# Performance work log

Measured on AMD Instinct MI355X. Metric: run time of the kernel, lower is better.

The kernel has to match this reference:

```python
import jax, jax.numpy as jnp
import numpy as np

EPS = 1e-5

def _pairwise_sq_dist(x, e):
    # x: [N, D], e: [M, D] -> [N, M]; matches torch.addmm(||e||^2 + ||x||^2, x, e.T, alpha=-2, beta=1)
    return (jnp.sum(e * e, axis=1)[None, :]
            + jnp.sum(x * x, axis=1, keepdims=True)
            - 2.0 * (x @ e.T))

def _dist2ph(d, t):
    # softmax(-sqrt(d)/t); clamp tiny negative numerical residues before sqrt
    return jax.nn.softmax(-jnp.sqrt(jnp.maximum(d, 0.0)) / t, axis=-1)

def setup_inputs() -> dict:
    key = jax.random.key(0)
    k1, k2, k3 = jax.random.split(key, 3)
    B, T, D, M = 64, 128, 256, 1024
    audio_semantic = jax.random.normal(k1, (B, T, D), dtype=jnp.float32)
    video_semantic = jax.random.normal(k2, (B, T, D), dtype=jnp.float32)
    init_bound = 1.0 / 400.0
    embedding = jax.random.uniform(k3, (M, D), dtype=jnp.float32,
                                   minval=-init_bound, maxval=init_bound)
    return {"audio_semantic": audio_semantic,
            "video_semantic": video_semantic,
            "embedding": embedding}

def reference(audio_semantic, video_semantic, embedding):
    B, T, D = audio_semantic.shape
    M = embedding.shape[0]
    emb_sg = jax.lax.stop_gradient(embedding)

    # ---- VQ argmin + straight-through quantize (Audio/Video_vq_embedding) ----
    a_flat_sg = jax.lax.stop_gradient(audio_semantic).reshape(-1, D)
    v_flat_sg = jax.lax.stop_gradient(video_semantic).reshape(-1, D)
    a_idx = jnp.argmin(_pairwise_sq_dist(a_flat_sg, emb_sg), axis=-1)  # [B*T]
    v_idx = jnp.argmin(_pairwise_sq_dist(v_flat_sg, emb_sg), axis=-1)
    a_quantized = audio_semantic + jax.lax.stop_gradient(
        emb_sg[a_idx].reshape(B, T, D) - audio_semantic)
    v_quantized = video_semantic + jax.lax.stop_gradient(
        emb_sg[v_idx].reshape(B, T, D) - video_semantic)

    # ---- entropy-weighted cross-modal contrastive loss (cmcm_loss) ----
    a_dg = _pairwise_sq_dist(audio_semantic.reshape(-1, D), embedding)  # [B*T, M], grads flow
    v_dg = _pairwise_sq_dist(video_semantic.reshape(-1, D), embedding)

    a_pH = _dist2ph(a_dg, 1.0).reshape(B, T, M).transpose(1, 0, 2)     # [T, B, M]
    v_pH = _dist2ph(v_dg, 1.0).reshape(B, T, M).transpose(1, 0, 2)
    a_adj_ph = _dist2ph(a_dg, 0.5).reshape(B, T, M).transpose(1, 0, 2)
    v_adj_ph = _dist2ph(v_dg, 0.5).reshape(B, T, M).transpose(1, 0, 2)

    def cmcm(p_adj, q):
        # Scode[t] = p_adj[t] @ log(q[t]).T  -> [T, B, B]
        S = jnp.einsum('tbm,tcm->tbc', p_adj, jnp.log(q + 1e-10))
        S = S + jnp.max(-S)                 # matches MaxScode = max(-Scode)
        E = jnp.exp(S)
        diag = jnp.diagonal(E, axis1=-2, axis2=-1)          # [T, B]
        return -jnp.mean(jnp.log(diag / (jnp.sum(E, axis=-1) + EPS)))

    Lcmcm = cmcm(a_adj_ph, v_pH)
    Lcmcm2 = cmcm(v_adj_ph, a_pH)
    cmcm_loss = 0.5 * (Lcmcm + Lcmcm2)
    return cmcm_loss, a_quantized, v_quantized
```

## Files before the change

kernel.cpp:

```cpp
#include <hip/hip_runtime.h>

#define NROWS 8192
#define MCB   1024
#define DD    256
#define TT    128
#define BB    64

#define OFF_DA      0ul
#define OFF_DV      8388608ul
#define OFF_XX_A    16777216ul
#define OFF_XX_V    16785408ul
#define OFF_EE      16793600ul
#define OFF_SMIN_A  16794624ul
#define OFF_LZ1_A   16802816ul
#define OFF_IZ2_A   16811008ul
#define OFF_IDX_A   16819200ul
#define OFF_SMIN_V  16827392ul
#define OFF_LZ1_V   16835584ul
#define OFF_IZ2_V   16843776ul
#define OFF_IDX_V   16851968ul
#define OFF_S1      16860160ul
#define OFF_S2      17384448ul
#define OFF_PART    17908736ul
#define OFF_MAX     17908992ul
#define OFF_PACC    17909000ul
#define OFF_HIA     17909504ul
#define OFF_LOA     (OFF_HIA + 1048576ul)
#define OFF_HIV     (OFF_HIA + 2097152ul)
#define OFF_LOV     (OFF_HIA + 3145728ul)
#define OFF_HIE     (OFF_HIA + 4194304ul)
#define OFF_LOE     (OFF_HIE + 131072ul)

typedef __attribute__((ext_vector_type(8))) short bf16x8;
typedef __attribute__((ext_vector_type(4))) float f32x4;

__device__ __forceinline__ void gload_lds16u(const ushort* gsrc, ushort* ldst) {
  __builtin_amdgcn_global_load_lds(
      (const __attribute__((address_space(1))) void*)gsrc,
      (__attribute__((address_space(3))) void*)ldst, 16, 0, 0);
}
__device__ __forceinline__ ushort bf16_rne(float x) {
  unsigned u = __float_as_uint(x);
  unsigned r = u + 0x7FFFu + ((u >> 16) & 1u);
  return (ushort)(r >> 16);
}
__device__ __forceinline__ float bf16_f(ushort h) {
  return __uint_as_float((unsigned)h << 16);
}

__global__ void k_sumsq(const float* __restrict__ A, const float* __restrict__ V,
                        const float* __restrict__ E, float* __restrict__ ws) {
  const int lane = threadIdx.x & 63;
  const int wid  = threadIdx.x >> 6;
  const int row = blockIdx.x * 4 + wid;
  const float* src; float* dst; ushort* hi; ushort* lo; int r;
  if (row < 8192)       { src = A; r = row;         dst = ws + OFF_XX_A;
                          hi = (ushort*)(ws + OFF_HIA); lo = (ushort*)(ws + OFF_LOA); }
  else if (row < 16384) { src = V; r = row - 8192;  dst = ws + OFF_XX_V;
                          hi = (ushort*)(ws + OFF_HIV); lo = (ushort*)(ws + OFF_LOV); }
  else                  { src = E; r = row - 16384; dst = ws + OFF_EE;
                          hi = (ushort*)(ws + OFF_HIE); lo = (ushort*)(ws + OFF_LOE); }
  float4 x = *(const float4*)(src + (size_t)r * DD + lane * 4);
  ushort4 h, l;
  h.x = bf16_rne(x.x); l.x = bf16_rne(x.x - bf16_f(h.x));
  h.y = bf16_rne(x.y); l.y = bf16_rne(x.y - bf16_f(h.y));
  h.z = bf16_rne(x.z); l.z = bf16_rne(x.z - bf16_f(h.z));
  h.w = bf16_rne(x.w); l.w = bf16_rne(x.w - bf16_f(h.w));
  *(ushort4*)(hi + (size_t)r * DD + lane * 4) = h;
  *(ushort4*)(lo + (size_t)r * DD + lane * 4) = l;
  double acc = (double)x.x * x.x + (double)x.y * x.y +
               (double)x.z * x.z + (double)x.w * x.w;
  #pragma unroll
  for (int off = 32; off; off >>= 1) acc += __shfl_xor(acc, off);
  if (lane == 0) dst[r] = (float)acc;
}

__global__ __launch_bounds__(256) void k_dist(const float* __restrict__ A,
    const float* __restrict__ V, const float* __restrict__ E,
    float* __restrict__ ws) {
  const int z = blockIdx.z;
  const ushort* Xhi = (const ushort*)(ws + (z ? OFF_HIV : OFF_HIA));
  const ushort* Xlo = (const ushort*)(ws + (z ? OFF_LOV : OFF_LOA));
  const ushort* Ehi = (const ushort*)(ws + OFF_HIE);
  const ushort* Elo = (const ushort*)(ws + OFF_LOE);
  const float* xx = ws + (z ? OFF_XX_V : OFF_XX_A);
  const float* ee = ws + OFF_EE;
  float* Dst = ws + (z ? OFF_DV : OFF_DA);

  __shared__ __align__(16) ushort LAhi[128 * 32];
  __shared__ __align__(16) ushort LAlo[128 * 32];
  __shared__ __align__(16) ushort LBhi[128 * 32];
  __shared__ __align__(16) ushort LBlo[128 * 32];

  const int tid = threadIdx.x;
  const int bid = blockIdx.y * 8 + blockIdx.x;
  const int sw  = (bid & 7) * 64 + (bid >> 3);
  const int colb = sw & 7, rowb = sw >> 3;
  const int row0 = rowb * 128;
  const int col0 = colb * 128;

  const int wv = tid >> 6, lane = tid & 63;
  const int wr = wv >> 1, wc = wv & 1;
  const int rl = lane & 15, kg = lane >> 4;

  const int c0 = tid, c1 = 256 + tid;
  const int r0 = c0 >> 2, lg0 = (c0 & 3) ^ ((r0 >> 1) & 3);
  const int r1 = c1 >> 2, lg1 = (c1 & 3) ^ ((r1 >> 1) & 3);
  const ushort* gAhi0 = Xhi + (size_t)(row0 + r0) * DD + lg0 * 8;
  const ushort* gAhi1 = Xhi + (size_t)(row0 + r1) * DD + lg1 * 8;
  const ushort* gAlo0 = Xlo + (size_t)(row0 + r0) * DD + lg0 * 8;
  const ushort* gAlo1 = Xlo + (size_t)(row0 + r1) * DD + lg1 * 8;
  const ushort* gBhi0 = Ehi + (size_t)(col0 + r0) * DD + lg0 * 8;
  const ushort* gBhi1 = Ehi + (size_t)(col0 + r1) * DD + lg1 * 8;
  const ushort* gBlo0 = Elo + (size_t)(col0 + r0) * DD + lg0 * 8;
  const ushort* gBlo1 = Elo + (size_t)(col0 + r1) * DD + lg1 * 8;
  const int d0 = c0 * 8, d1 = c1 * 8;

  int aidx[4], bidx[4];
  #pragma unroll
  for (int f = 0; f < 4; ++f) {
    int ra = wr * 64 + f * 16 + rl;
    aidx[f] = ra * 32 + ((kg ^ ((ra >> 1) & 3)) << 3);
    int rb = wc * 64 + f * 16 + rl;
    bidx[f] = rb * 32 + ((kg ^ ((rb >> 1) & 3)) << 3);
  }

  f32x4 acc[4][4] = {};

  for (int t = 0; t < 8; ++t) {
    const int kc = t * 32;
    gload_lds16u(gAhi0 + kc, &LAhi[d0]);
    gload_lds16u(gAhi1 + kc, &LAhi[d1]);
    gload_lds16u(gAlo0 + kc, &LAlo[d0]);
    gload_lds16u(gAlo1 + kc, &LAlo[d1]);
    gload_lds16u(gBhi0 + kc, &LBhi[d0]);
    gload_lds16u(gBhi1 + kc, &LBhi[d1]);
    gload_lds16u(gBlo0 + kc, &LBlo[d0]);
    gload_lds16u(gBlo1 + kc, &LBlo[d1]);
    __syncthreads();
    __builtin_amdgcn_s_setprio(1);
    bf16x8 ahi[4], alo[4], bhi[4], blo[4];
    #pragma unroll
    for (int f = 0; f < 4; ++f) {
      ahi[f] = *(const bf16x8*)(&LAhi[aidx[f]]);
      alo[f] = *(const bf16x8*)(&LAlo[aidx[f]]);
      bhi[f] = *(const bf16x8*)(&LBhi[bidx[f]]);
      blo[f] = *(const bf16x8*)(&LBlo[bidx[f]]);
    }
    #pragma unroll
    for (int fr = 0; fr < 4; ++fr)
      #pragma unroll
      for (int fc = 0; fc < 4; ++fc) {
        acc[fr][fc] = __builtin_amdgcn_mfma_f32_16x16x32_bf16(
            ahi[fr], bhi[fc], acc[fr][fc], 0, 0, 0);
        acc[fr][fc] = __builtin_amdgcn_mfma_f32_16x16x32_bf16(
            ahi[fr], blo[fc], acc[fr][fc], 0, 0, 0);
        acc[fr][fc] = __builtin_amdgcn_mfma_f32_16x16x32_bf16(
            alo[fr], bhi[fc], acc[fr][fc], 0, 0, 0);
      }
    __builtin_amdgcn_s_setprio(0);
    __syncthreads();
  }

  float xn[4][4];
  #pragma unroll
  for (int fr = 0; fr < 4; ++fr)
    #pragma unroll
    for (int v = 0; v < 4; ++v)
      xn[fr][v] = xx[row0 + wr * 64 + fr * 16 + kg * 4 + v];
  #pragma unroll
  for (int fc = 0; fc < 4; ++fc) {
    const int m = col0 + wc * 64 + fc * 16 + rl;
    const float em = ee[m];
    #pragma unroll
    for (int fr = 0; fr < 4; ++fr) {
      #pragma unroll
      for (int v = 0; v < 4; ++v) {
        const int n = row0 + wr * 64 + fr * 16 + kg * 4 + v;
        Dst[(size_t)n * MCB + m] = (em + xn[fr][v]) - 2.0f * acc[fr][fc][v];
      }
    }
  }
}

__global__ void k_rowstats(const float* __restrict__ A, const float* __restrict__ V,
                           const float* __restrict__ E, float* __restrict__ ws,
                           float* __restrict__ out) {
  const int z = blockIdx.y;
  float* Dm = ws + (z ? OFF_DV : OFF_DA);
  const float* X  = z ? V : A;
  float* smin_o = ws + (z ? OFF_SMIN_V : OFF_SMIN_A);
  float* lz1_o  = ws + (z ? OFF_LZ1_V  : OFF_LZ1_A);
  float* iz2_o  = ws + (z ? OFF_IZ2_V  : OFF_IZ2_A);
  int*   idx_o  = (int*)(ws + (z ? OFF_IDX_V : OFF_IDX_A));
  float* qout = out + 1 + (size_t)z * ((size_t)NROWS * DD);

  const int lane = threadIdx.x & 63, wid = threadIdx.x >> 6;
  const int n = blockIdx.x * 4 + wid;
  float* drow = Dm + (size_t)n * MCB;

  float v[16];
  #pragma unroll
  for (int c = 0; c < 4; ++c) {
    float4 t = *(const float4*)(drow + c * 256 + lane * 4);
    v[c*4+0] = t.x; v[c*4+1] = t.y; v[c*4+2] = t.z; v[c*4+3] = t.w;
  }
  float bv = 3.4e38f; int bi = 0;
  #pragma unroll
  for (int c = 0; c < 4; ++c)
    #pragma unroll
    for (int j = 0; j < 4; ++j) {
      float val = v[c*4+j];
      int m = c * 256 + lane * 4 + j;
      if (val < bv) { bv = val; bi = m; }
    }
  #pragma unroll
  for (int off = 32; off; off >>= 1) {
    float ov = __shfl_xor(bv, off);
    int   oi = __shfl_xor(bi, off);
    if (ov < bv || (ov == bv && oi < bi)) { bv = ov; bi = oi; }
  }
  float smin = sqrtf(fmaxf(bv, 0.0f));
  float w[16], e2[16];
  float z1 = 0.f, z2 = 0.f;
  #pragma unroll
  for (int q = 0; q < 16; ++q) {
    w[q] = sqrtf(fmaxf(v[q], 0.0f)) - smin;
    z1 += __expf(-w[q]);
    e2[q] = __expf(-2.0f * w[q]);
    z2 += e2[q];
  }
  #pragma unroll
  for (int off = 32; off; off >>= 1) {
    z1 += __shfl_xor(z1, off);
    z2 += __shfl_xor(z2, off);
  }
  if (lane == 0) {
    smin_o[n] = smin;
    lz1_o[n]  = __logf(z1);
    iz2_o[n]  = 1.0f / z2;
    idx_o[n]  = bi;
  }
  ushort* prow = (ushort*)drow;
  #pragma unroll
  for (int c = 0; c < 4; ++c) {
    ushort4 hp, hw;
    hp.x = bf16_rne(e2[c*4+0]); hp.y = bf16_rne(e2[c*4+1]);
    hp.z = bf16_rne(e2[c*4+2]); hp.w = bf16_rne(e2[c*4+3]);
    hw.x = bf16_rne(w[c*4+0]);  hw.y = bf16_rne(w[c*4+1]);
    hw.z = bf16_rne(w[c*4+2]);  hw.w = bf16_rne(w[c*4+3]);
    *(ushort4*)(prow + c * 256 + lane * 4) = hp;
    *(ushort4*)(prow + 1024 + c * 256 + lane * 4) = hw;
  }
  const float* erow = E + (size_t)bi * DD;
  const float* xrow = X + (size_t)n * DD;
  #pragma unroll
  for (int p = 0; p < 4; ++p) {
    int dd = p * 64 + lane;
    float xv = xrow[dd];
    float ev = erow[dd];
    qout[(size_t)n * DD + dd] = xv + (ev - xv);
  }
}

__global__ __launch_bounds__(512) void k_sgemm(float* __restrict__ ws) {
  const int z = blockIdx.y;
  const int t = blockIdx.x;
  const ushort* P = (const ushort*)(ws + (z ? OFF_DV : OFF_DA));
  const ushort* Q = (const ushort*)(ws + (z ? OFF_DA : OFF_DV));
  const float* iz2_p  = ws + (z ? OFF_IZ2_V  : OFF_IZ2_A);
  const float* lz1_q  = ws + (z ? OFF_LZ1_A  : OFF_LZ1_V);
  float* S = ws + (z ? OFF_S2 : OFF_S1);
  float* part = ws + OFF_PART;

  __shared__ __align__(16) ushort PAs[2][64 * 64];
  __shared__ __align__(16) ushort WQs[2][64 * 64];
  __shared__ float redmin[8];

  const int tid = threadIdx.x;
  const int wv = tid >> 6, lane = tid & 63;
  const int rl = lane & 15, kg = lane >> 4;
  const int bt  = (wv & 3) * 16;
  const int ctl = (wv >> 2) * 32;

  const int sr = tid >> 3, sg = tid & 7;
  const int lg = sg ^ (sr & 7);
  const ushort* gP = P + (size_t)(sr * TT + t) * 2048 + lg * 8;
  const ushort* gQ = Q + (size_t)(sr * TT + t) * 2048 + 1024 + lg * 8;
  const int dso = tid * 8;

  const int ra = bt + rl;
  const int rb0 = ctl + rl, rb1 = ctl + 16 + rl;
  int aoff[2], b0off[2], b1off[2];
  #pragma unroll
  for (int ks = 0; ks < 2; ++ks) {
    int g = ks * 4 + kg;
    aoff[ks]  = ra  * 64 + ((g ^ (ra  & 7)) * 8);
    b0off[ks] = rb0 * 64 + ((g ^ (rb0 & 7)) * 8);
    b1off[ks] = rb1 * 64 + ((g ^ (rb1 & 7)) * 8);
  }

  f32x4 acc0 = {}, acc1 = {};

  gload_lds16u(gP, &PAs[0][dso]);
  gload_lds16u(gQ, &WQs[0][dso]);
  __syncthreads();

  for (int ch = 0; ch < 16; ++ch) {
    const int cur = ch & 1;
    if (ch < 15) {
      gload_lds16u(gP + (ch + 1) * 64, &PAs[cur ^ 1][dso]);
      gload_lds16u(gQ + (ch + 1) * 64, &WQs[cur ^ 1][dso]);
    }
    __builtin_amdgcn_s_setprio(1);
    #pragma unroll
    for (int ks = 0; ks < 2; ++ks) {
      bf16x8 af = *(const bf16x8*)(&PAs[cur][aoff[ks]]);
      bf16x8 b0 = *(const bf16x8*)(&WQs[cur][b0off[ks]]);
      bf16x8 b1 = *(const bf16x8*)(&WQs[cur][b1off[ks]]);
      acc0 = __builtin_amdgcn_mfma_f32_16x16x32_bf16(af, b0, acc0, 0, 0, 0);
      acc1 = __builtin_amdgcn_mfma_f32_16x16x32_bf16(af, b1, acc1, 0, 0, 0);
    }
    __builtin_amdgcn_s_setprio(0);
    __syncthreads();
  }

  const float lzq0 = lz1_q[(size_t)rb0 * TT + t];
  const float lzq1 = lz1_q[(size_t)rb1 * TT + t];
  float mn = 3.4e38f;
  #pragma unroll
  for (int v = 0; v < 4; ++v) {
    const int b = bt + kg * 4 + v;
    const float izb = iz2_p[(size_t)b * TT + t];
    float s0 = -izb * acc0[v] - lzq0;
    float s1 = -izb * acc1[v] - lzq1;
    S[((size_t)t * 64 + b) * 64 + rb0] = s0;
    S[((size_t)t * 64 + b) * 64 + rb1] = s1;
    mn = fminf(mn, fminf(s0, s1));
  }
  #pragma unroll
  for (int off = 32; off; off >>= 1) mn = fminf(mn, __shfl_xor(mn, off));
  if (lane == 0) redmin[wv] = mn;
  __syncthreads();
  if (tid == 0) {
    float m = redmin[0];
    #pragma unroll
    for (int i = 1; i < 8; ++i) m = fminf(m, redmin[i]);
    part[z * 128 + t] = m;
  }
}

__global__ void k_sfinal(float* __restrict__ ws) {
  const float* part = ws + OFF_PART;
  float* maxv = ws + OFF_MAX;
  const int tens = threadIdx.x >> 7;
  const int i = threadIdx.x & 127;
  float m = part[tens * 128 + i];
  #pragma unroll
  for (int off = 32; off; off >>= 1) m = fminf(m, __shfl_xor(m, off));
  __shared__ float red[4];
  const int lane = threadIdx.x & 63, wid = threadIdx.x >> 6;
  if (lane == 0) red[wid] = m;
  __syncthreads();
  if (threadIdx.x == 0)   maxv[0] = -fminf(red[0], red[1]);
  if (threadIdx.x == 128) maxv[1] = -fminf(red[2], red[3]);
}

__global__ __launch_bounds__(256) void k_loss(float* __restrict__ ws) {
  const int lane = threadIdx.x & 63, wid = threadIdx.x >> 6;
  const int wglobal = blockIdx.x * 4 + wid;
  const float* Smax = ws + OFF_MAX;
  double acc = 0.0;
  #pragma unroll 4
  for (int r = 0; r < 16; ++r) {
    int gw = wglobal * 16 + r;
    int tens = gw >> 13;
    int rem = gw & 8191;
    const float* S = ws + (tens ? OFF_S2 : OFF_S1);
    float maxv = Smax[tens];
    float ev = __expf(S[(size_t)rem * 64 + lane] + maxv);
    float sum = ev;
    #pragma unroll
    for (int off = 32; off; off >>= 1) sum += __shfl_xor(sum, off);
    float diag = __shfl(ev, rem & 63);
    if (lane == 0) acc += (double)__logf(diag / (sum + 1e-5f));
  }
  __shared__ double red[4];
  if (lane == 0) red[wid] = acc;
  __syncthreads();
  if (threadIdx.x == 0)
    ((double*)(ws + OFF_PACC))[blockIdx.x] = red[0] + red[1] + red[2] + red[3];
}

__global__ void k_fin(const float* __restrict__ ws, float* __restrict__ out) {
  const double* p = (const double*)(ws + OFF_PACC);
  const int lane = threadIdx.x & 63, wid = threadIdx.x >> 6;
  double v = p[threadIdx.x];
  #pragma unroll
  for (int off = 32; off; off >>= 1) v += __shfl_xor(v, off);
  __shared__ double red[4];
  if (lane == 0) red[wid] = v;
  __syncthreads();
  if (threadIdx.x == 0)
    out[0] = (float)(-(red[0] + red[1] + red[2] + red[3]) / 16384.0);
}

extern "C" void kernel_launch(void* const* d_in, const int* in_sizes, int n_in,
                              void* d_out, int out_size, void* d_ws, size_t ws_size,
                              hipStream_t stream) {
  const float* A = (const float*)d_in[0];
  const float* V = (const float*)d_in[1];
  const float* E = (const float*)d_in[2];
  float* out = (float*)d_out;
  float* ws  = (float*)d_ws;

  k_sumsq  <<<dim3(4352), dim3(256), 0, stream>>>(A, V, E, ws);
  k_dist   <<<dim3(8, 64, 2), dim3(256), 0, stream>>>(A, V, E, ws);
  k_rowstats<<<dim3(2048, 2), dim3(256), 0, stream>>>(A, V, E, ws, out);
  k_sgemm  <<<dim3(128, 2), dim3(512), 0, stream>>>(ws);
  k_sfinal <<<dim3(1), dim3(256), 0, stream>>>(ws);
  k_loss   <<<dim3(256), dim3(256), 0, stream>>>(ws);
  k_fin    <<<dim3(1), dim3(256), 0, stream>>>(ws, out);
}
```

Measured before the change: 98.54 us.

## Load S-GEMM operands straight into registers and fold max reduction into loss kernel

The S-GEMM kernel stops staging P and Q tiles through double-buffered LDS with barriers. Each wave now loads its bf16 fragments directly from global memory into registers and feeds the MFMAs, with the loop unrolled. The single-block k_sfinal kernel is removed, and every k_loss block recomputes the global max from the 256 partial minima before its main loop, which saves one launch. In exchange, the same operands are read redundantly by several waves with less coalesced accesses, and each loss block repeats a small reduction.

```diff
diff --git a/kernel.cpp b/kernel.cpp
--- a/kernel.cpp
+++ b/kernel.cpp
@@ -273,8 +273,6 @@
   float* S = ws + (z ? OFF_S2 : OFF_S1);
   float* part = ws + OFF_PART;
 
-  __shared__ __align__(16) ushort PAs[2][64 * 64];
-  __shared__ __align__(16) ushort WQs[2][64 * 64];
   __shared__ float redmin[8];
 
   const int tid = threadIdx.x;
@@ -283,46 +281,27 @@
   const int bt  = (wv & 3) * 16;
   const int ctl = (wv >> 2) * 32;
 
-  const int sr = tid >> 3, sg = tid & 7;
-  const int lg = sg ^ (sr & 7);
-  const ushort* gP = P + (size_t)(sr * TT + t) * 2048 + lg * 8;
-  const ushort* gQ = Q + (size_t)(sr * TT + t) * 2048 + 1024 + lg * 8;
-  const int dso = tid * 8;
-
-  const int ra = bt + rl;
+  const int ra  = bt + rl;
   const int rb0 = ctl + rl, rb1 = ctl + 16 + rl;
-  int aoff[2], b0off[2], b1off[2];
-  #pragma unroll
-  for (int ks = 0; ks < 2; ++ks) {
-    int g = ks * 4 + kg;
-    aoff[ks]  = ra  * 64 + ((g ^ (ra  & 7)) * 8);
-    b0off[ks] = rb0 * 64 + ((g ^ (rb0 & 7)) * 8);
-    b1off[ks] = rb1 * 64 + ((g ^ (rb1 & 7)) * 8);
-  }
+  const ushort* pa_b = P + ((size_t)ra  * TT + t) * 2048 + kg * 8;
+  const ushort* wq0b = Q + ((size_t)rb0 * TT + t) * 2048 + 1024 + kg * 8;
+  const ushort* wq1b = Q + ((size_t)rb1 * TT + t) * 2048 + 1024 + kg * 8;
 
   f32x4 acc0 = {}, acc1 = {};
 
-  gload_lds16u(gP, &PAs[0][dso]);
-  gload_lds16u(gQ, &WQs[0][dso]);
-  __syncthreads();
-
+  #pragma unroll 4
   for (int ch = 0; ch < 16; ++ch) {
-    const int cur = ch & 1;
-    if (ch < 15) {
-      gload_lds16u(gP + (ch + 1) * 64, &PAs[cur ^ 1][dso]);
-      gload_lds16u(gQ + (ch + 1) * 64, &WQs[cur ^ 1][dso]);
-    }
-    __builtin_amdgcn_s_setprio(1);
-    #pragma unroll
-    for (int ks = 0; ks < 2; ++ks) {
-      bf16x8 af = *(const bf16x8*)(&PAs[cur][aoff[ks]]);
-      bf16x8 b0 = *(const bf16x8*)(&WQs[cur][b0off[ks]]);
-      bf16x8 b1 = *(const bf16x8*)(&WQs[cur][b1off[ks]]);
-      acc0 = __builtin_amdgcn_mfma_f32_16x16x32_bf16(af, b0, acc0, 0, 0, 0);
-      acc1 = __builtin_amdgcn_mfma_f32_16x16x32_bf16(af, b1, acc1, 0, 0, 0);
-    }
-    __builtin_amdgcn_s_setprio(0);
-    __syncthreads();
+    const int off = ch * 64;
+    bf16x8 a0  = *(const bf16x8*)(pa_b + off);
+    bf16x8 a1  = *(const bf16x8*)(pa_b + off + 32);
+    bf16x8 b00 = *(const bf16x8*)(wq0b + off);
+    bf16x8 b01 = *(const bf16x8*)(wq0b + off + 32);
+    bf16x8 b10 = *(const bf16x8*)(wq1b + off);
+    bf16x8 b11 = *(const bf16x8*)(wq1b + off + 32);
+    acc0 = __builtin_amdgcn_mfma_f32_16x16x32_bf16(a0, b00, acc0, 0, 0, 0);
+    acc1 = __builtin_amdgcn_mfma_f32_16x16x32_bf16(a0, b10, acc1, 0, 0, 0);
+    acc0 = __builtin_amdgcn_mfma_f32_16x16x32_bf16(a1, b01, acc0, 0, 0, 0);
+    acc1 = __builtin_amdgcn_mfma_f32_16x16x32_bf16(a1, b11, acc1, 0, 0, 0);
   }
 
   const float lzq0 = lz1_q[(size_t)rb0 * TT + t];
@@ -350,26 +329,21 @@
   }
 }
 
-__global__ void k_sfinal(float* __restrict__ ws) {
-  const float* part = ws + OFF_PART;
-  float* maxv = ws + OFF_MAX;
-  const int tens = threadIdx.x >> 7;
-  const int i = threadIdx.x & 127;
-  float m = part[tens * 128 + i];
-  #pragma unroll
-  for (int off = 32; off; off >>= 1) m = fminf(m, __shfl_xor(m, off));
-  __shared__ float red[4];
-  const int lane = threadIdx.x & 63, wid = threadIdx.x >> 6;
-  if (lane == 0) red[wid] = m;
-  __syncthreads();
-  if (threadIdx.x == 0)   maxv[0] = -fminf(red[0], red[1]);
-  if (threadIdx.x == 128) maxv[1] = -fminf(red[2], red[3]);
-}
-
 __global__ __launch_bounds__(256) void k_loss(float* __restrict__ ws) {
   const int lane = threadIdx.x & 63, wid = threadIdx.x >> 6;
+  const float* part = ws + OFF_PART;
+  __shared__ float red[4];
+  __shared__ float smax[2];
+  float m = part[threadIdx.x];
+  #pragma unroll
+  for (int off = 32; off; off >>= 1) m = fminf(m, __shfl_xor(m, off));
+  if (lane == 0) red[wid] = m;
+  __syncthreads();
+  if (threadIdx.x == 0)   smax[0] = -fminf(red[0], red[1]);
+  if (threadIdx.x == 128) smax[1] = -fminf(red[2], red[3]);
+  __syncthreads();
+
   const int wglobal = blockIdx.x * 4 + wid;
-  const float* Smax = ws + OFF_MAX;
   double acc = 0.0;
   #pragma unroll 4
   for (int r = 0; r < 16; ++r) {
@@ -377,7 +351,7 @@
     int tens = gw >> 13;
     int rem = gw & 8191;
     const float* S = ws + (tens ? OFF_S2 : OFF_S1);
-    float maxv = Smax[tens];
+    float maxv = smax[tens];
     float ev = __expf(S[(size_t)rem * 64 + lane] + maxv);
     float sum = ev;
     #pragma unroll
@@ -385,11 +359,11 @@
     float diag = __shfl(ev, rem & 63);
     if (lane == 0) acc += (double)__logf(diag / (sum + 1e-5f));
   }
-  __shared__ double red[4];
-  if (lane == 0) red[wid] = acc;
+  __shared__ double dred[4];
+  if (lane == 0) dred[wid] = acc;
   __syncthreads();
   if (threadIdx.x == 0)
-    ((double*)(ws + OFF_PACC))[blockIdx.x] = red[0] + red[1] + red[2] + red[3];
+    ((double*)(ws + OFF_PACC))[blockIdx.x] = dred[0] + dred[1] + dred[2] + dred[3];
 }
 
 __global__ void k_fin(const float* __restrict__ ws, float* __restrict__ out) {
@@ -418,7 +392,6 @@
   k_dist   <<<dim3(8, 64, 2), dim3(256), 0, stream>>>(A, V, E, ws);
   k_rowstats<<<dim3(2048, 2), dim3(256), 0, stream>>>(A, V, E, ws, out);
   k_sgemm  <<<dim3(128, 2), dim3(512), 0, stream>>>(ws);
-  k_sfinal <<<dim3(1), dim3(256), 0, stream>>>(ws);
   k_loss   <<<dim3(256), dim3(256), 0, stream>>>(ws);
   k_fin    <<<dim3(1), dim3(256), 0, stream>>>(ws, out);
 }
```

Result: slower. 108.3 us (+9.9%).
